# Performance work log

Hardware: AMD Instinct MI355X
Metric: run time of the kernel (lower is better)

## Reference

```python
import jax, jax.numpy as jnp
import numpy as np

N = 100000        # nodes
E = 1600000       # edges (avg degree 16)
IN = 128          # in_channels
HID = 256         # hidden_channels
OUT = 2           # out_channels
G = 512           # num graphs in batch


def setup_inputs() -> dict:
    key = jax.random.key(0)
    ks = jax.random.split(key, 10)
    x = jax.random.normal(ks[0], (N, IN), dtype=jnp.float32)
    edge_index = jax.random.randint(ks[1], (2, E), 0, N, dtype=jnp.int64)
    # sorted graph assignment, every graph non-empty (PyG-style batching)
    batch = (jnp.arange(N, dtype=jnp.int64) * G) // N
    s = 1.0 / np.sqrt(IN)
    sh = 1.0 / np.sqrt(2 * HID)
    sh1 = 1.0 / np.sqrt(HID)
    W_l = jax.random.uniform(ks[2], (HID, IN), jnp.float32, -s, s)   # SAGE lin_l (neighbors)
    b_l = jax.random.uniform(ks[3], (HID,), jnp.float32, -s, s)
    W_r = jax.random.uniform(ks[4], (HID, IN), jnp.float32, -s, s)   # SAGE lin_r (root), no bias
    W0 = jax.random.uniform(ks[5], (HID, IN), jnp.float32, -s, s)    # lin0
    b0 = jax.random.uniform(ks[5], (HID,), jnp.float32, -s, s)
    W1 = jax.random.uniform(ks[6], (HID, 2 * HID), jnp.float32, -sh, sh)  # lin1
    b1 = jax.random.uniform(ks[7], (HID,), jnp.float32, -sh, sh)
    W2 = jax.random.uniform(ks[8], (OUT, HID), jnp.float32, -sh1, sh1)    # lin2
    b2 = jax.random.uniform(ks[9], (OUT,), jnp.float32, -sh1, sh1)
    return {"x": x, "edge_index": edge_index, "batch": batch,
            "W_l": W_l, "b_l": b_l, "W_r": W_r,
            "W0": W0, "b0": b0, "W1": W1, "b1": b1, "W2": W2, "b2": b2}


def reference(x, edge_index, batch, W_l, b_l, W_r, W0, b0, W1, b1, W2, b2):
    src, dst = edge_index[0], edge_index[1]
    # SAGEConv: mean-aggregate neighbor features (gather -> scatter-add -> normalize)
    msg_sum = jax.ops.segment_sum(x[src], dst, num_segments=N)          # [N, IN]
    deg = jax.ops.segment_sum(jnp.ones((E,), x.dtype), dst, num_segments=N)
    aggr = msg_sum / jnp.maximum(deg, 1.0)[:, None]
    h = jax.nn.relu(aggr @ W_l.T + b_l + x @ W_r.T)                     # [N, HID]
    # global max pool per graph
    hp = jax.ops.segment_max(h, batch, num_segments=G)                  # [G, HID]
    # root node = first node of each graph (batch is sorted)
    root = jnp.searchsorted(batch, jnp.arange(G, dtype=batch.dtype))    # [G]
    news = jax.nn.relu(x[root] @ W0.T + b0)                             # [G, HID]
    h = jax.nn.relu(jnp.concatenate([news, hp], axis=-1) @ W1.T + b1)   # [G, HID]
    h = h @ W2.T + b2                                                   # [G, OUT]
    return jax.nn.log_softmax(h, axis=-1)
```

## Files before the change

kernel.cpp:

```cpp
#include <hip/hip_runtime.h>
#include <hip/hip_bf16.h>
#include <math.h>
#include <stdint.h>

#define IN_C 128
#define HID  256
#define OUT_C 2

#define BSHIFT 9
#define BNODES 512
#define EPB 4096

typedef __attribute__((ext_vector_type(8))) short short8;
typedef __attribute__((ext_vector_type(4))) float f32x4;
typedef __attribute__((ext_vector_type(2))) float f32x2;

#if defined(__has_builtin)
#if __has_builtin(__builtin_amdgcn_cvt_pk_f32_fp8) && __has_builtin(__builtin_amdgcn_cvt_pk_fp8_f32)
#define HAVE_FP8_CVT 1
#endif
#if __has_builtin(__builtin_amdgcn_global_load_lds)
#define HAVE_GLL 1
#endif
#endif

__device__ __forceinline__ ushort f2bf(float f) {
  uint32_t u = __float_as_uint(f);
  uint32_t r = u + 0x7FFF + ((u >> 16) & 1);
  return (ushort)(r >> 16);
}
__device__ __forceinline__ float bf2f(ushort b) {
  return __uint_as_float(((uint32_t)b) << 16);
}

#ifndef HAVE_FP8_CVT
__device__ __forceinline__ uint32_t f2fp8_1(float f) {
  uint32_t u = __float_as_uint(f);
  uint32_t s = (u >> 24) & 0x80;
  float a = fabsf(f);
  if (a >= 448.f) return s | 0x7E;
  if (a < 0.015625f) {
    uint32_t m = (uint32_t)(a * 512.f + 0.5f);
    return s | m;
  }
  uint32_t r = u & 0x7fffffff;
  r += 0x7FFFF + ((r >> 20) & 1);
  uint32_t e = (r >> 23) - 127;
  if ((int)e > 8) return s | 0x7E;
  return s | ((e + 7) << 3) | ((r >> 20) & 7);
}
__device__ __forceinline__ float fp8_2f(uint32_t b) {
  uint32_t s = (b & 0x80) << 24;
  uint32_t e = (b >> 3) & 0xF, m = b & 7;
  if (e == 0) { float f = (float)m * 0.001953125f; return s ? -f : f; }
  return __uint_as_float(s | ((e + 120) << 23) | (m << 20));
}
#endif

__device__ __forceinline__ void acc8f8v(f32x2* s, uint2 v) {
#ifdef HAVE_FP8_CVT
  s[0] += __builtin_amdgcn_cvt_pk_f32_fp8(v.x, false);
  s[1] += __builtin_amdgcn_cvt_pk_f32_fp8(v.x, true);
  s[2] += __builtin_amdgcn_cvt_pk_f32_fp8(v.y, false);
  s[3] += __builtin_amdgcn_cvt_pk_f32_fp8(v.y, true);
#else
  s[0].x += fp8_2f(v.x & 0xff);         s[0].y += fp8_2f((v.x >> 8) & 0xff);
  s[1].x += fp8_2f((v.x >> 16) & 0xff); s[1].y += fp8_2f(v.x >> 24);
  s[2].x += fp8_2f(v.y & 0xff);         s[2].y += fp8_2f((v.y >> 8) & 0xff);
  s[3].x += fp8_2f((v.y >> 16) & 0xff); s[3].y += fp8_2f(v.y >> 24);
#endif
}


__global__ void k_hist(const int* __restrict__ dst, int* __restrict__ bcount, int E) {
  __shared__ int h[256];
  int t = threadIdx.x;
  h[t] = 0;
  __syncthreads();
  for (int e = blockIdx.x * 256 + t; e < E; e += gridDim.x * 256)
    atomicAdd(&h[dst[e] >> BSHIFT], 1);
  __syncthreads();
  if (h[t]) atomicAdd(&bcount[t], h[t]);
}

__global__ void k_bucket_scan(const int* __restrict__ bcount,
                              int* __restrict__ bbase, int* __restrict__ bcursor) {
  __shared__ int sd[256];
  int t = threadIdx.x;
  int cnt = bcount[t];
  sd[t] = cnt;
  __syncthreads();
  for (int off = 1; off < 256; off <<= 1) {
    int v = (t >= off) ? sd[t - off] : 0;
    __syncthreads();
    sd[t] += v;
    __syncthreads();
  }
  int base = sd[t] - cnt;
  bbase[t] = base;
  bcursor[t] = base;
}

__global__ __launch_bounds__(256) void k_scatter(
    const int* __restrict__ src, const int* __restrict__ dst,
    int* __restrict__ bcursor, uint32_t* __restrict__ rec, int E) {
  __shared__ int h[256];
  __shared__ int bbase[256];
  __shared__ int lcur[256];
  int t = threadIdx.x;
  int e0 = blockIdx.x * EPB;
  int e1 = e0 + EPB < E ? e0 + EPB : E;
  h[t] = 0; lcur[t] = 0;
  __syncthreads();
  for (int e = e0 + t; e < e1; e += 256)
    atomicAdd(&h[dst[e] >> BSHIFT], 1);
  __syncthreads();
  if (h[t]) bbase[t] = atomicAdd(&bcursor[t], h[t]);
  __syncthreads();
  for (int e = e0 + t; e < e1; e += 256) {
    int d = dst[e];
    int b = d >> BSHIFT;
    int r = atomicAdd(&lcur[b], 1);
    rec[bbase[b] + r] = ((uint32_t)src[e] << BSHIFT) | ((uint32_t)d & (BNODES - 1));
  }
}

__global__ __launch_bounds__(256) void k_csr(
    const uint32_t* __restrict__ rec, const int* __restrict__ bbase,
    const int* __restrict__ bcount,
    int* __restrict__ row_start, int* __restrict__ deg,
    int* __restrict__ csr, int n) {
  __shared__ int ldeg[BNODES];
  __shared__ int lexcl[BNODES];
  __shared__ int ssum[256];
  int t = threadIdx.x;
  int b = blockIdx.x;
  int node0 = b << BSHIFT;
  int ebase = bbase[b];
  int ecnt = bcount[b];

  ldeg[t] = 0; ldeg[t + 256] = 0;
  __syncthreads();
  for (int i = t; i < ecnt; i += 256)
    atomicAdd(&ldeg[rec[ebase + i] & (BNODES - 1)], 1);
  __syncthreads();

  int v0 = ldeg[2 * t], v1 = ldeg[2 * t + 1];
  ssum[t] = v0 + v1;
  __syncthreads();
  for (int off = 1; off < 256; off <<= 1) {
    int v = (t >= off) ? ssum[t - off] : 0;
    __syncthreads();
    ssum[t] += v;
    __syncthreads();
  }
  int excl = ssum[t] - (v0 + v1);
  lexcl[2 * t] = excl;
  lexcl[2 * t + 1] = excl + v0;
  int node = node0 + 2 * t;
  if (node < n) { row_start[node] = ebase + excl; deg[node] = v0; }
  if (node + 1 < n) { row_start[node + 1] = ebase + excl + v0; deg[node + 1] = v1; }
  ldeg[2 * t] = 0; ldeg[2 * t + 1] = 0;
  __syncthreads();
  for (int i = t; i < ecnt; i += 256) {
    uint32_t r = rec[ebase + i];
    int li = r & (BNODES - 1);
    int k = atomicAdd(&ldeg[li], 1);
    csr[ebase + lexcl[li] + k] = (int)(r >> BSHIFT);
  }
}


__global__ void k_prep(const float* __restrict__ x, ushort* __restrict__ xb,
                       uint32_t* __restrict__ xf8, int n4,
                       const float* __restrict__ Wl, const float* __restrict__ Wr,
                       ushort* __restrict__ Wcat,
                       const float* __restrict__ W0, ushort* __restrict__ W0b,
                       const float* __restrict__ W1, ushort* __restrict__ W1b,
                       const int* __restrict__ batch, int* __restrict__ root, int n) {
  int i = blockIdx.x * 256 + threadIdx.x;
  if (i < n4) {
    float4 v = ((const float4*)x)[i];
    ushort4 o = {f2bf(v.x), f2bf(v.y), f2bf(v.z), f2bf(v.w)};
    ((ushort4*)xb)[i] = o;
#ifdef HAVE_FP8_CVT
    int p = __builtin_amdgcn_cvt_pk_fp8_f32(v.x, v.y, 0, false);
    p = __builtin_amdgcn_cvt_pk_fp8_f32(v.z, v.w, p, true);
    xf8[i] = (uint32_t)p;
#else
    xf8[i] = f2fp8_1(v.x) | (f2fp8_1(v.y) << 8) | (f2fp8_1(v.z) << 16) |
             (f2fp8_1(v.w) << 24);
#endif
  }
  if (i < HID * (2 * IN_C) / 4) {
    int c = i >> 6, c4 = (i & 63) * 4;
    float4 v = (c4 < IN_C) ? *(const float4*)(Wl + (size_t)c * IN_C + c4)
                           : *(const float4*)(Wr + (size_t)c * IN_C + (c4 - IN_C));
    ushort4 o = {f2bf(v.x), f2bf(v.y), f2bf(v.z), f2bf(v.w)};
    *(ushort4*)(Wcat + (size_t)c * (2 * IN_C) + c4) = o;
  }
  if (i < HID * IN_C / 4) {
    float4 v = ((const float4*)W0)[i];
    ushort4 o = {f2bf(v.x), f2bf(v.y), f2bf(v.z), f2bf(v.w)};
    ((ushort4*)W0b)[i] = o;
  }
  if (i < HID * 2 * HID / 4) {
    float4 v = ((const float4*)W1)[i];
    ushort4 o = {f2bf(v.x), f2bf(v.y), f2bf(v.z), f2bf(v.w)};
    ((ushort4*)W1b)[i] = o;
  }
  if (i < n) {
    int g = batch[i];
    if (i == 0 || batch[i - 1] != g) root[g] = i;
  }
}


__global__ void k_aggr(const uint32_t* __restrict__ xf8, const int* __restrict__ csr,
                       const int* __restrict__ row_start, const int* __restrict__ deg,
                       ushort* __restrict__ aggr, int n) {
  int wid = threadIdx.x >> 6;
  int lane = threadIdx.x & 63;
  int node = blockIdx.x * 4 + wid;
  if (node >= n) return;
  int base = row_start[node];
  int d = deg[node];
  int q = lane >> 4, li = lane & 15;
  const uint2* xp = (const uint2*)xf8 + li;
  f32x2 s[4] = {};
  int i = q;
  for (; i + 12 < d; i += 16) {
    int n0 = csr[base + i];
    int n1 = csr[base + i + 4];
    int n2 = csr[base + i + 8];
    int n3 = csr[base + i + 12];
    uint2 a = xp[(size_t)n0 * 16];
    uint2 b = xp[(size_t)n1 * 16];
    uint2 c = xp[(size_t)n2 * 16];
    uint2 e = xp[(size_t)n3 * 16];
    acc8f8v(s, a); acc8f8v(s, b); acc8f8v(s, c); acc8f8v(s, e);
  }
  for (; i < d; i += 4) {
    int n0 = csr[base + i];
    uint2 a = xp[(size_t)n0 * 16];
    acc8f8v(s, a);
  }
#pragma unroll
  for (int j = 0; j < 4; ++j) {
    s[j].x += __shfl_xor(s[j].x, 16); s[j].y += __shfl_xor(s[j].y, 16);
    s[j].x += __shfl_xor(s[j].x, 32); s[j].y += __shfl_xor(s[j].y, 32);
  }
  if (q == 0) {
    float inv = 1.0f / (float)(d > 1 ? d : 1);
    uint4 o;
    o.x = (uint32_t)f2bf(s[0].x * inv) | ((uint32_t)f2bf(s[0].y * inv) << 16);
    o.y = (uint32_t)f2bf(s[1].x * inv) | ((uint32_t)f2bf(s[1].y * inv) << 16);
    o.z = (uint32_t)f2bf(s[2].x * inv) | ((uint32_t)f2bf(s[2].y * inv) << 16);
    o.w = (uint32_t)f2bf(s[3].x * inv) | ((uint32_t)f2bf(s[3].y * inv) << 16);
    ((uint4*)(aggr + (size_t)node * IN_C))[li] = o;
  }
}


#ifdef HAVE_GLL
__device__ __forceinline__ void load16_lds(const ushort* g, ushort* l) {
  __builtin_amdgcn_global_load_lds(
      (const __attribute__((address_space(1))) uint32_t*)g,
      (__attribute__((address_space(3))) uint32_t*)l, 16, 0, 0);
}
#endif

__global__ __launch_bounds__(256) void k_gemm_pool(
    const ushort* __restrict__ aggrb, const ushort* __restrict__ xb,
    const ushort* __restrict__ Wcat, const float* __restrict__ bl,
    const int* __restrict__ batch, float* __restrict__ hp, int n) {
  __shared__ ushort sA[64 * 256];
  __shared__ float sbl[256];
  __shared__ int sBatch[64];

  int t = threadIdx.x;
  int n0 = blockIdx.x * 64;
  sbl[t] = bl[t];
  if (t < 64) sBatch[t] = (n0 + t < n) ? batch[n0 + t] : -1;

  int lane = t & 63, w = t >> 6;
  int q = lane >> 4, m = lane & 15;

#pragma unroll
  for (int j = 0; j < 8; ++j) {
    int s = (j * 4 + w) * 64 + lane;
    int r = s >> 5, p = s & 31;
    int c = p ^ (r & 15);
    int gn = n0 + r; gn = gn < n ? gn : n - 1;
    const ushort* g = (c < 16) ? aggrb + (size_t)gn * IN_C + c * 8
                               : xb + (size_t)gn * IN_C + (c - 16) * 8;
#ifdef HAVE_GLL
    load16_lds(g, &sA[(size_t)s * 8]);
#else
    *(uint4*)&sA[(size_t)s * 8] = *(const uint4*)g;
#endif
  }

  short8 bf_n[4];
#pragma unroll
  for (int ct = 0; ct < 4; ++ct)
    bf_n[ct] = *(const short8*)(Wcat + (size_t)(w * 64 + ct * 16 + m) * (2 * IN_C) + q * 8);

  __syncthreads();

  f32x4 acc[4][4] = {};
#pragma unroll
  for (int kc = 0; kc < 8; ++kc) {
    short8 bf[4];
#pragma unroll
    for (int ct = 0; ct < 4; ++ct) bf[ct] = bf_n[ct];
    if (kc < 7) {
#pragma unroll
      for (int ct = 0; ct < 4; ++ct)
        bf_n[ct] = *(const short8*)(Wcat + (size_t)(w * 64 + ct * 16 + m) * (2 * IN_C) +
                                    (kc + 1) * 32 + q * 8);
    }
    short8 af[4];
#pragma unroll
    for (int rt = 0; rt < 4; ++rt) {
      int r = rt * 16 + m;
      int p = (kc * 4 + q) ^ m;
      af[rt] = *(const short8*)&sA[r * 256 + p * 8];
    }
#pragma unroll
    for (int rt = 0; rt < 4; ++rt)
#pragma unroll
      for (int ct = 0; ct < 4; ++ct)
        acc[rt][ct] = __builtin_amdgcn_mfma_f32_16x16x32_bf16(af[rt], bf[ct], acc[rt][ct], 0, 0, 0);
  }

  int last = n - 1 - n0; last = last < 63 ? last : 63;
  int gA = sBatch[0];
  int gB = sBatch[last];
#pragma unroll
  for (int ct = 0; ct < 4; ++ct) {
    int col = w * 64 + ct * 16 + m;
    float bias = sbl[col];
    float mA = 0.f, mB = 0.f;
#pragma unroll
    for (int rt = 0; rt < 4; ++rt) {
#pragma unroll
      for (int i = 0; i < 4; ++i) {
        int lr = rt * 16 + q * 4 + i;
        if (n0 + lr < n) {
          float v = fmaxf(acc[rt][ct][i] + bias, 0.f);
          if (sBatch[lr] == gA) mA = fmaxf(mA, v);
          else mB = fmaxf(mB, v);
        }
      }
    }
    mA = fmaxf(mA, __shfl_xor(mA, 16)); mA = fmaxf(mA, __shfl_xor(mA, 32));
    mB = fmaxf(mB, __shfl_xor(mB, 16)); mB = fmaxf(mB, __shfl_xor(mB, 32));
    if (q == 0) {
      atomicMax((int*)&hp[(size_t)gA * HID + col], __float_as_int(mA));
      if (gB != gA) atomicMax((int*)&hp[(size_t)gB * HID + col], __float_as_int(mB));
    }
  }
}


__global__ __launch_bounds__(256) void k_tail(
    const ushort* __restrict__ xb, const float* __restrict__ hp,
    const int* __restrict__ root,
    const ushort* __restrict__ W0b, const float* __restrict__ b0,
    const ushort* __restrict__ W1b, const float* __restrict__ b1,
    const float* __restrict__ W2, const float* __restrict__ b2,
    float* __restrict__ out, int G) {
  __shared__ ushort sCat[64][264];
  __shared__ int sRoot[64];
  __shared__ float pp[256][2];

  int t = threadIdx.x;
  int g0 = blockIdx.x * 64;
  if (t < 64) sRoot[t] = (g0 + t < G) ? root[g0 + t] : 0;
  __syncthreads();

  int lane = t & 63, w = t >> 6;
  int q = lane >> 4, m = lane & 15;

  const ushort* xrow[4];
#pragma unroll
  for (int rt = 0; rt < 4; ++rt)
    xrow[rt] = xb + (size_t)sRoot[rt * 16 + m] * IN_C;

  {
    f32x4 acc[4][4] = {};
#pragma unroll
    for (int kc = 0; kc < 4; ++kc) {
      short8 af[4], bf[4];
#pragma unroll
      for (int rt = 0; rt < 4; ++rt)
        af[rt] = *(const short8*)(xrow[rt] + kc * 32 + q * 8);
#pragma unroll
      for (int ct = 0; ct < 4; ++ct) {
        int col = w * 64 + ct * 16 + m;
        bf[ct] = *(const short8*)(W0b + (size_t)col * IN_C + kc * 32 + q * 8);
      }
#pragma unroll
      for (int rt = 0; rt < 4; ++rt)
#pragma unroll
        for (int ct = 0; ct < 4; ++ct)
          acc[rt][ct] = __builtin_amdgcn_mfma_f32_16x16x32_bf16(af[rt], bf[ct], acc[rt][ct], 0, 0, 0);
    }
#pragma unroll
    for (int ct = 0; ct < 4; ++ct) {
      int col = w * 64 + ct * 16 + m;
      float bias = b0[col];
#pragma unroll
      for (int rt = 0; rt < 4; ++rt)
#pragma unroll
        for (int i = 0; i < 4; ++i) {
          int row = rt * 16 + q * 4 + i;
          sCat[row][col] = f2bf(fmaxf(acc[rt][ct][i] + bias, 0.f));
        }
    }
  }
  __syncthreads();

  f32x4 acc2[4][4] = {};
#pragma unroll
  for (int kc = 0; kc < 8; ++kc) {
    short8 af[4], bf[4];
#pragma unroll
    for (int rt = 0; rt < 4; ++rt)
      af[rt] = *(const short8*)&sCat[rt * 16 + m][kc * 32 + q * 8];
#pragma unroll
    for (int ct = 0; ct < 4; ++ct) {
      int col = w * 64 + ct * 16 + m;
      bf[ct] = *(const short8*)(W1b + (size_t)col * (2 * HID) + kc * 32 + q * 8);
    }
#pragma unroll
    for (int rt = 0; rt < 4; ++rt)
#pragma unroll
      for (int ct = 0; ct < 4; ++ct)
        acc2[rt][ct] = __builtin_amdgcn_mfma_f32_16x16x32_bf16(af[rt], bf[ct], acc2[rt][ct], 0, 0, 0);
  }
  __syncthreads();
#pragma unroll
  for (int it = 0; it < 16; ++it) {
    int idx = it * 256 + t;
    int r = idx >> 6, c4 = (idx & 63) * 4;
    if (g0 + r < G) {
      float4 v = *(const float4*)(hp + (size_t)(g0 + r) * HID + c4);
      ushort4 o = {f2bf(v.x), f2bf(v.y), f2bf(v.z), f2bf(v.w)};
      *(ushort4*)&sCat[r][c4] = o;
    }
  }
  __syncthreads();
#pragma unroll
  for (int kc = 8; kc < 16; ++kc) {
    short8 af[4], bf[4];
#pragma unroll
    for (int rt = 0; rt < 4; ++rt)
      af[rt] = *(const short8*)&sCat[rt * 16 + m][(kc - 8) * 32 + q * 8];
#pragma unroll
    for (int ct = 0; ct < 4; ++ct) {
      int col = w * 64 + ct * 16 + m;
      bf[ct] = *(const short8*)(W1b + (size_t)col * (2 * HID) + kc * 32 + q * 8);
    }
#pragma unroll
    for (int rt = 0; rt < 4; ++rt)
#pragma unroll
      for (int ct = 0; ct < 4; ++ct)
        acc2[rt][ct] = __builtin_amdgcn_mfma_f32_16x16x32_bf16(af[rt], bf[ct], acc2[rt][ct], 0, 0, 0);
  }
  __syncthreads();
#pragma unroll
  for (int ct = 0; ct < 4; ++ct) {
    int col = w * 64 + ct * 16 + m;
    float bias = b1[col];
#pragma unroll
    for (int rt = 0; rt < 4; ++rt)
#pragma unroll
      for (int i = 0; i < 4; ++i) {
        int row = rt * 16 + q * 4 + i;
        sCat[row][col] = f2bf(fmaxf(acc2[rt][ct][i] + bias, 0.f));
      }
  }
  __syncthreads();

  {
    int row = t >> 2, qq = t & 3;
    float p0 = 0.f, p1 = 0.f;
    for (int c = qq * 64; c < qq * 64 + 64; ++c) {
      float hv = bf2f(sCat[row][c]);
      p0 += hv * W2[c];
      p1 += hv * W2[HID + c];
    }
    pp[t][0] = p0; pp[t][1] = p1;
  }
  __syncthreads();
  if (t < 64 && g0 + t < G) {
    float l0 = b2[0], l1 = b2[1];
#pragma unroll
    for (int k = 0; k < 4; ++k) { l0 += pp[t * 4 + k][0]; l1 += pp[t * 4 + k][1]; }
    float mx = fmaxf(l0, l1);
    float ls = logf(expf(l0 - mx) + expf(l1 - mx));
    out[(size_t)(g0 + t) * 2 + 0] = l0 - mx - ls;
    out[(size_t)(g0 + t) * 2 + 1] = l1 - mx - ls;
  }
}


extern "C" void kernel_launch(void* const* d_in, const int* in_sizes, int n_in,
                              void* d_out, int out_size, void* d_ws, size_t ws_size,
                              hipStream_t stream) {
  const float* x  = (const float*)d_in[0];
  const int* ei   = (const int*)d_in[1];
  const int* batch= (const int*)d_in[2];
  const float* Wl = (const float*)d_in[3];
  const float* bl = (const float*)d_in[4];
  const float* Wr = (const float*)d_in[5];
  const float* W0 = (const float*)d_in[6];
  const float* b0 = (const float*)d_in[7];
  const float* W1 = (const float*)d_in[8];
  const float* b1 = (const float*)d_in[9];
  const float* W2 = (const float*)d_in[10];
  const float* b2 = (const float*)d_in[11];
  float* out = (float*)d_out;

  const int N = in_sizes[0] / IN_C;
  const int E = in_sizes[1] / 2;
  const int G = out_size / OUT_C;
  const int* src = ei;
  const int* dst = ei + E;
  const int NB = (N + BNODES - 1) >> BSHIFT;

  char* w = (char*)d_ws;
  int* deg       = (int*)w; w += (size_t)N * 4;
  int* row_start = (int*)w; w += (size_t)N * 4;
  int* bcount    = (int*)w; w += 1024;
  int* bbase     = (int*)w; w += 1024;
  int* bcursor   = (int*)w; w += 1024;
  int* root      = (int*)w; w += (size_t)G * 4;
  w = (char*)(((uintptr_t)w + 255) & ~(uintptr_t)255);
  int* csr       = (int*)w; w += (size_t)E * 4;
  w = (char*)(((uintptr_t)w + 255) & ~(uintptr_t)255);
  ushort* xb     = (ushort*)w; w += (size_t)N * IN_C * 2;
  uint32_t* xf8  = (uint32_t*)w; w += (size_t)N * IN_C;
  ushort* aggrb  = (ushort*)w; w += (size_t)N * IN_C * 2;
  ushort* Wcat   = (ushort*)w; w += (size_t)HID * (2 * IN_C) * 2;
  ushort* W0b    = (ushort*)w; w += (size_t)HID * IN_C * 2;
  ushort* W1b    = (ushort*)w; w += (size_t)HID * 2 * HID * 2;
  float* hp      = (float*)w; w += (size_t)G * HID * 4;
  uint32_t* rec  = (uint32_t*)aggrb;

  hipMemsetAsync(bcount, 0, 1024, stream);
  hipMemsetAsync(hp, 0, (size_t)G * HID * 4, stream);

  int n4 = N * IN_C / 4;
  k_prep<<<(n4 + 255) / 256, 256, 0, stream>>>(x, xb, xf8, n4, Wl, Wr, Wcat,
                                               W0, W0b, W1, W1b, batch, root, N);
  k_hist<<<1024, 256, 0, stream>>>(dst, bcount, E);
  k_bucket_scan<<<1, 256, 0, stream>>>(bcount, bbase, bcursor);
  k_scatter<<<(E + EPB - 1) / EPB, 256, 0, stream>>>(src, dst, bcursor, rec, E);
  k_csr<<<NB, 256, 0, stream>>>(rec, bbase, bcount, row_start, deg, csr, N);
  k_aggr<<<(N + 3) / 4, 256, 0, stream>>>(xf8, csr, row_start, deg, aggrb, N);
  k_gemm_pool<<<(N + 63) / 64, 256, 0, stream>>>(aggrb, xb, Wcat, bl, batch, hp, N);
  k_tail<<<(G + 63) / 64, 256, 0, stream>>>(xb, hp, root, W0b, b0, W1b, b1, W2, b2, out, G);
}
```

Baseline: 299.9 us.

## Fuse histogram into prep, pad CSR rows, shrink tail tiles

```diff
diff --git a/kernel.cpp b/kernel.cpp
--- a/kernel.cpp
+++ b/kernel.cpp
@@ -7,9 +7,11 @@
 #define HID  256
 #define OUT_C 2
 
-#define BSHIFT 9
-#define BNODES 512
+#define BSHIFT 8
+#define BNODES 256
 #define EPB 4096
+#define HISTB 784
+#define PADB 3840
 
 typedef __attribute__((ext_vector_type(8))) short short8;
 typedef __attribute__((ext_vector_type(4))) float f32x4;
@@ -72,113 +74,18 @@
 }
 
 
-__global__ void k_hist(const int* __restrict__ dst, int* __restrict__ bcount, int E) {
-  __shared__ int h[256];
-  int t = threadIdx.x;
-  h[t] = 0;
-  __syncthreads();
-  for (int e = blockIdx.x * 256 + t; e < E; e += gridDim.x * 256)
-    atomicAdd(&h[dst[e] >> BSHIFT], 1);
-  __syncthreads();
-  if (h[t]) atomicAdd(&bcount[t], h[t]);
-}
-
-__global__ void k_bucket_scan(const int* __restrict__ bcount,
-                              int* __restrict__ bbase, int* __restrict__ bcursor) {
-  __shared__ int sd[256];
-  int t = threadIdx.x;
-  int cnt = bcount[t];
-  sd[t] = cnt;
-  __syncthreads();
-  for (int off = 1; off < 256; off <<= 1) {
-    int v = (t >= off) ? sd[t - off] : 0;
-    __syncthreads();
-    sd[t] += v;
-    __syncthreads();
-  }
-  int base = sd[t] - cnt;
-  bbase[t] = base;
-  bcursor[t] = base;
-}
-
-__global__ __launch_bounds__(256) void k_scatter(
-    const int* __restrict__ src, const int* __restrict__ dst,
-    int* __restrict__ bcursor, uint32_t* __restrict__ rec, int E) {
-  __shared__ int h[256];
-  __shared__ int bbase[256];
-  __shared__ int lcur[256];
-  int t = threadIdx.x;
-  int e0 = blockIdx.x * EPB;
-  int e1 = e0 + EPB < E ? e0 + EPB : E;
-  h[t] = 0; lcur[t] = 0;
-  __syncthreads();
-  for (int e = e0 + t; e < e1; e += 256)
-    atomicAdd(&h[dst[e] >> BSHIFT], 1);
-  __syncthreads();
-  if (h[t]) bbase[t] = atomicAdd(&bcursor[t], h[t]);
-  __syncthreads();
-  for (int e = e0 + t; e < e1; e += 256) {
-    int d = dst[e];
-    int b = d >> BSHIFT;
-    int r = atomicAdd(&lcur[b], 1);
-    rec[bbase[b] + r] = ((uint32_t)src[e] << BSHIFT) | ((uint32_t)d & (BNODES - 1));
-  }
-}
-
-__global__ __launch_bounds__(256) void k_csr(
-    const uint32_t* __restrict__ rec, const int* __restrict__ bbase,
-    const int* __restrict__ bcount,
-    int* __restrict__ row_start, int* __restrict__ deg,
-    int* __restrict__ csr, int n) {
-  __shared__ int ldeg[BNODES];
-  __shared__ int lexcl[BNODES];
-  __shared__ int ssum[256];
-  int t = threadIdx.x;
-  int b = blockIdx.x;
-  int node0 = b << BSHIFT;
-  int ebase = bbase[b];
-  int ecnt = bcount[b];
-
-  ldeg[t] = 0; ldeg[t + 256] = 0;
-  __syncthreads();
-  for (int i = t; i < ecnt; i += 256)
-    atomicAdd(&ldeg[rec[ebase + i] & (BNODES - 1)], 1);
-  __syncthreads();
-
-  int v0 = ldeg[2 * t], v1 = ldeg[2 * t + 1];
-  ssum[t] = v0 + v1;
-  __syncthreads();
-  for (int off = 1; off < 256; off <<= 1) {
-    int v = (t >= off) ? ssum[t - off] : 0;
-    __syncthreads();
-    ssum[t] += v;
-    __syncthreads();
-  }
-  int excl = ssum[t] - (v0 + v1);
-  lexcl[2 * t] = excl;
-  lexcl[2 * t + 1] = excl + v0;
-  int node = node0 + 2 * t;
-  if (node < n) { row_start[node] = ebase + excl; deg[node] = v0; }
-  if (node + 1 < n) { row_start[node + 1] = ebase + excl + v0; deg[node + 1] = v1; }
-  ldeg[2 * t] = 0; ldeg[2 * t + 1] = 0;
-  __syncthreads();
-  for (int i = t; i < ecnt; i += 256) {
-    uint32_t r = rec[ebase + i];
-    int li = r & (BNODES - 1);
-    int k = atomicAdd(&ldeg[li], 1);
-    csr[ebase + lexcl[li] + k] = (int)(r >> BSHIFT);
-  }
-}
-
-
 __global__ void k_prep(const float* __restrict__ x, ushort* __restrict__ xb,
                        uint32_t* __restrict__ xf8, int n4,
                        const float* __restrict__ Wl, const float* __restrict__ Wr,
                        ushort* __restrict__ Wcat,
                        const float* __restrict__ W0, ushort* __restrict__ W0b,
                        const float* __restrict__ W1, ushort* __restrict__ W1b,
-                       const int* __restrict__ batch, int* __restrict__ root, int n) {
-  int i = blockIdx.x * 256 + threadIdx.x;
+                       const int* __restrict__ batch, int* __restrict__ root, int n,
+                       const int* __restrict__ dst, int E, int* __restrict__ bcount,
+                       float* __restrict__ hp, int hp4) {
+  __shared__ int h[512];
+  int t = threadIdx.x;
+  int i = blockIdx.x * 256 + t;
   if (i < n4) {
     float4 v = ((const float4*)x)[i];
     ushort4 o = {f2bf(v.x), f2bf(v.y), f2bf(v.z), f2bf(v.w)};
@@ -192,6 +99,7 @@
              (f2fp8_1(v.w) << 24);
 #endif
   }
+  if (i < 32) xf8[(size_t)n * 32 + i] = 0;
   if (i < HID * (2 * IN_C) / 4) {
     int c = i >> 6, c4 = (i & 63) * 4;
     float4 v = (c4 < IN_C) ? *(const float4*)(Wl + (size_t)c * IN_C + c4)
@@ -209,10 +117,117 @@
     ushort4 o = {f2bf(v.x), f2bf(v.y), f2bf(v.z), f2bf(v.w)};
     ((ushort4*)W1b)[i] = o;
   }
+  if (i < hp4) ((float4*)hp)[i] = make_float4(0.f, 0.f, 0.f, 0.f);
   if (i < n) {
     int g = batch[i];
     if (i == 0 || batch[i - 1] != g) root[g] = i;
   }
+  if (blockIdx.x < HISTB) {
+    h[t] = 0; h[t + 256] = 0;
+    __syncthreads();
+    for (int e = blockIdx.x * 256 + t; e < E; e += HISTB * 256)
+      atomicAdd(&h[dst[e] >> BSHIFT], 1);
+    __syncthreads();
+    if (h[t]) atomicAdd(&bcount[t], h[t]);
+    if (h[t + 256]) atomicAdd(&bcount[t + 256], h[t + 256]);
+  }
+}
+
+
+__global__ __launch_bounds__(256) void k_scatter(
+    const int* __restrict__ src, const int* __restrict__ dst,
+    const int* __restrict__ bcount, int* __restrict__ cursor0,
+    uint32_t* __restrict__ rec, int E) {
+  __shared__ int sBB[512];
+  __shared__ int stmp[256];
+  __shared__ int h[512];
+  __shared__ int hb[512];
+  __shared__ int lcur[512];
+  int t = threadIdx.x;
+  int c0 = bcount[2 * t], c1 = bcount[2 * t + 1];
+  stmp[t] = c0 + c1;
+  h[2 * t] = 0; h[2 * t + 1] = 0;
+  lcur[2 * t] = 0; lcur[2 * t + 1] = 0;
+  __syncthreads();
+  for (int off = 1; off < 256; off <<= 1) {
+    int v = (t >= off) ? stmp[t - off] : 0;
+    __syncthreads();
+    stmp[t] += v;
+    __syncthreads();
+  }
+  int ex = stmp[t] - (c0 + c1);
+  sBB[2 * t] = ex;
+  sBB[2 * t + 1] = ex + c0;
+  __syncthreads();
+
+  int e0 = blockIdx.x * EPB;
+  int e1 = e0 + EPB < E ? e0 + EPB : E;
+  for (int e = e0 + t; e < e1; e += 256)
+    atomicAdd(&h[dst[e] >> BSHIFT], 1);
+  __syncthreads();
+  for (int j = t; j < 512; j += 256)
+    if (h[j]) hb[j] = sBB[j] + atomicAdd(&cursor0[j], h[j]);
+  __syncthreads();
+  for (int e = e0 + t; e < e1; e += 256) {
+    int d = dst[e];
+    int b = d >> BSHIFT;
+    int r = atomicAdd(&lcur[b], 1);
+    rec[hb[b] + r] = ((uint32_t)src[e] << BSHIFT) | ((uint32_t)d & (BNODES - 1));
+  }
+}
+
+
+__global__ __launch_bounds__(256) void k_csr(
+    const uint32_t* __restrict__ rec, const int* __restrict__ bcount,
+    int* __restrict__ row_start, int* __restrict__ deg,
+    int* __restrict__ csr, int n, int zrow) {
+  __shared__ int stmp[256];
+  __shared__ int lexcl[256];
+  __shared__ int ldeg[256];
+  __shared__ int lcur[256];
+  int t = threadIdx.x, b = blockIdx.x;
+  int i2 = 2 * t;
+  int v = ((i2 < b) ? bcount[i2] : 0) + ((i2 + 1 < b) ? bcount[i2 + 1] : 0);
+  stmp[t] = v;
+  ldeg[t] = 0;
+  __syncthreads();
+  for (int off = 128; off > 0; off >>= 1) {
+    if (t < off) stmp[t] += stmp[t + off];
+    __syncthreads();
+  }
+  int ebase = stmp[0];
+  int ecnt = bcount[b];
+  int padbase = ((ebase + 15) & ~15) + PADB * b;
+  int node0 = b << BSHIFT;
+  __syncthreads();
+
+  for (int i = t; i < ecnt; i += 256)
+    atomicAdd(&ldeg[rec[ebase + i] & (BNODES - 1)], 1);
+  __syncthreads();
+  int d = ldeg[t];
+  int P = (d + 15) & ~15;
+  stmp[t] = P;
+  __syncthreads();
+  for (int off = 1; off < 256; off <<= 1) {
+    int vv = (t >= off) ? stmp[t - off] : 0;
+    __syncthreads();
+    stmp[t] += vv;
+    __syncthreads();
+  }
+  int excl = stmp[t] - P;
+  lexcl[t] = excl;
+  int rs = padbase + excl;
+  int node = node0 + t;
+  if (node < n) { row_start[node] = rs; deg[node] = d; }
+  lcur[t] = 0;
+  __syncthreads();
+  for (int i = t; i < ecnt; i += 256) {
+    uint32_t r = rec[ebase + i];
+    int li = r & (BNODES - 1);
+    int k = atomicAdd(&lcur[li], 1);
+    csr[padbase + lexcl[li] + k] = (int)(r >> BSHIFT);
+  }
+  for (int k = d; k < P; ++k) csr[rs + k] = zrow;
 }
 
 
@@ -225,25 +240,17 @@
   if (node >= n) return;
   int base = row_start[node];
   int d = deg[node];
+  int P = (d + 15) & ~15;
   int q = lane >> 4, li = lane & 15;
   const uint2* xp = (const uint2*)xf8 + li;
   f32x2 s[4] = {};
-  int i = q;
-  for (; i + 12 < d; i += 16) {
-    int n0 = csr[base + i];
-    int n1 = csr[base + i + 4];
-    int n2 = csr[base + i + 8];
-    int n3 = csr[base + i + 12];
-    uint2 a = xp[(size_t)n0 * 16];
-    uint2 b = xp[(size_t)n1 * 16];
-    uint2 c = xp[(size_t)n2 * 16];
-    uint2 e = xp[(size_t)n3 * 16];
+  for (int i = 4 * q; i < P; i += 16) {
+    int4 ns = *(const int4*)(csr + base + i);
+    uint2 a = xp[(size_t)ns.x * 16];
+    uint2 b = xp[(size_t)ns.y * 16];
+    uint2 c = xp[(size_t)ns.z * 16];
+    uint2 e = xp[(size_t)ns.w * 16];
     acc8f8v(s, a); acc8f8v(s, b); acc8f8v(s, c); acc8f8v(s, e);
-  }
-  for (; i < d; i += 4) {
-    int n0 = csr[base + i];
-    uint2 a = xp[(size_t)n0 * 16];
-    acc8f8v(s, a);
   }
 #pragma unroll
   for (int j = 0; j < 4; ++j) {
@@ -371,30 +378,30 @@
     const ushort* __restrict__ W1b, const float* __restrict__ b1,
     const float* __restrict__ W2, const float* __restrict__ b2,
     float* __restrict__ out, int G) {
-  __shared__ ushort sCat[64][264];
-  __shared__ int sRoot[64];
+  __shared__ ushort sCat[32][264];
+  __shared__ int sRoot[32];
   __shared__ float pp[256][2];
 
   int t = threadIdx.x;
-  int g0 = blockIdx.x * 64;
-  if (t < 64) sRoot[t] = (g0 + t < G) ? root[g0 + t] : 0;
+  int g0 = blockIdx.x * 32;
+  if (t < 32) sRoot[t] = (g0 + t < G) ? root[g0 + t] : 0;
   __syncthreads();
 
   int lane = t & 63, w = t >> 6;
   int q = lane >> 4, m = lane & 15;
 
-  const ushort* xrow[4];
-#pragma unroll
-  for (int rt = 0; rt < 4; ++rt)
+  const ushort* xrow[2];
+#pragma unroll
+  for (int rt = 0; rt < 2; ++rt)
     xrow[rt] = xb + (size_t)sRoot[rt * 16 + m] * IN_C;
 
   {
-    f32x4 acc[4][4] = {};
+    f32x4 acc[2][4] = {};
 #pragma unroll
     for (int kc = 0; kc < 4; ++kc) {
-      short8 af[4], bf[4];
-#pragma unroll
-      for (int rt = 0; rt < 4; ++rt)
+      short8 af[2], bf[4];
+#pragma unroll
+      for (int rt = 0; rt < 2; ++rt)
         af[rt] = *(const short8*)(xrow[rt] + kc * 32 + q * 8);
 #pragma unroll
       for (int ct = 0; ct < 4; ++ct) {
@@ -402,7 +409,7 @@
         bf[ct] = *(const short8*)(W0b + (size_t)col * IN_C + kc * 32 + q * 8);
       }
 #pragma unroll
-      for (int rt = 0; rt < 4; ++rt)
+      for (int rt = 0; rt < 2; ++rt)
 #pragma unroll
         for (int ct = 0; ct < 4; ++ct)
           acc[rt][ct] = __builtin_amdgcn_mfma_f32_16x16x32_bf16(af[rt], bf[ct], acc[rt][ct], 0, 0, 0);
@@ -412,7 +419,7 @@
       int col = w * 64 + ct * 16 + m;
       float bias = b0[col];
 #pragma unroll
-      for (int rt = 0; rt < 4; ++rt)
+      for (int rt = 0; rt < 2; ++rt)
 #pragma unroll
         for (int i = 0; i < 4; ++i) {
           int row = rt * 16 + q * 4 + i;
@@ -422,27 +429,34 @@
   }
   __syncthreads();
 
-  f32x4 acc2[4][4] = {};
+  f32x4 acc2[2][4] = {};
+  short8 bfn[4];
+#pragma unroll
+  for (int ct = 0; ct < 4; ++ct)
+    bfn[ct] = *(const short8*)(W1b + (size_t)(w * 64 + ct * 16 + m) * (2 * HID) + q * 8);
 #pragma unroll
   for (int kc = 0; kc < 8; ++kc) {
-    short8 af[4], bf[4];
-#pragma unroll
-    for (int rt = 0; rt < 4; ++rt)
+    short8 af[2], bf[4];
+#pragma unroll
+    for (int ct = 0; ct < 4; ++ct) bf[ct] = bfn[ct];
+    if (kc < 7) {
+#pragma unroll
+      for (int ct = 0; ct < 4; ++ct)
+        bfn[ct] = *(const short8*)(W1b + (size_t)(w * 64 + ct * 16 + m) * (2 * HID) +
+                                   (kc + 1) * 32 + q * 8);
+    }
+#pragma unroll
+    for (int rt = 0; rt < 2; ++rt)
       af[rt] = *(const short8*)&sCat[rt * 16 + m][kc * 32 + q * 8];
 #pragma unroll
-    for (int ct = 0; ct < 4; ++ct) {
-      int col = w * 64 + ct * 16 + m;
-      bf[ct] = *(const short8*)(W1b + (size_t)col * (2 * HID) + kc * 32 + q * 8);
-    }
-#pragma unroll
-    for (int rt = 0; rt < 4; ++rt)
+    for (int rt = 0; rt < 2; ++rt)
 #pragma unroll
       for (int ct = 0; ct < 4; ++ct)
         acc2[rt][ct] = __builtin_amdgcn_mfma_f32_16x16x32_bf16(af[rt], bf[ct], acc2[rt][ct], 0, 0, 0);
   }
   __syncthreads();
 #pragma unroll
-  for (int it = 0; it < 16; ++it) {
+  for (int it = 0; it < 8; ++it) {
     int idx = it * 256 + t;
     int r = idx >> 6, c4 = (idx & 63) * 4;
     if (g0 + r < G) {
@@ -453,18 +467,24 @@
   }
   __syncthreads();
 #pragma unroll
+  for (int ct = 0; ct < 4; ++ct)
+    bfn[ct] = *(const short8*)(W1b + (size_t)(w * 64 + ct * 16 + m) * (2 * HID) + 8 * 32 + q * 8);
+#pragma unroll
   for (int kc = 8; kc < 16; ++kc) {
-    short8 af[4], bf[4];
-#pragma unroll
-    for (int rt = 0; rt < 4; ++rt)
+    short8 af[2], bf[4];
+#pragma unroll
+    for (int ct = 0; ct < 4; ++ct) bf[ct] = bfn[ct];
+    if (kc < 15) {
+#pragma unroll
+      for (int ct = 0; ct < 4; ++ct)
+        bfn[ct] = *(const short8*)(W1b + (size_t)(w * 64 + ct * 16 + m) * (2 * HID) +
+                                   (kc + 1) * 32 + q * 8);
+    }
+#pragma unroll
+    for (int rt = 0; rt < 2; ++rt)
       af[rt] = *(const short8*)&sCat[rt * 16 + m][(kc - 8) * 32 + q * 8];
 #pragma unroll
-    for (int ct = 0; ct < 4; ++ct) {
-      int col = w * 64 + ct * 16 + m;
-      bf[ct] = *(const short8*)(W1b + (size_t)col * (2 * HID) + kc * 32 + q * 8);
-    }
-#pragma unroll
-    for (int rt = 0; rt < 4; ++rt)
+    for (int rt = 0; rt < 2; ++rt)
 #pragma unroll
       for (int ct = 0; ct < 4; ++ct)
         acc2[rt][ct] = __builtin_amdgcn_mfma_f32_16x16x32_bf16(af[rt], bf[ct], acc2[rt][ct], 0, 0, 0);
@@ -475,7 +495,7 @@
     int col = w * 64 + ct * 16 + m;
     float bias = b1[col];
 #pragma unroll
-    for (int rt = 0; rt < 4; ++rt)
+    for (int rt = 0; rt < 2; ++rt)
 #pragma unroll
       for (int i = 0; i < 4; ++i) {
         int row = rt * 16 + q * 4 + i;
@@ -485,9 +505,9 @@
   __syncthreads();
 
   {
-    int row = t >> 2, qq = t & 3;
+    int row = t >> 3, qq = t & 7;
     float p0 = 0.f, p1 = 0.f;
-    for (int c = qq * 64; c < qq * 64 + 64; ++c) {
+    for (int c = qq * 32; c < qq * 32 + 32; ++c) {
       float hv = bf2f(sCat[row][c]);
       p0 += hv * W2[c];
       p1 += hv * W2[HID + c];
@@ -495,10 +515,10 @@
     pp[t][0] = p0; pp[t][1] = p1;
   }
   __syncthreads();
-  if (t < 64 && g0 + t < G) {
+  if (t < 32 && g0 + t < G) {
     float l0 = b2[0], l1 = b2[1];
 #pragma unroll
-    for (int k = 0; k < 4; ++k) { l0 += pp[t * 4 + k][0]; l1 += pp[t * 4 + k][1]; }
+    for (int k = 0; k < 8; ++k) { l0 += pp[t * 8 + k][0]; l1 += pp[t * 8 + k][1]; }
     float mx = fmaxf(l0, l1);
     float ls = logf(expf(l0 - mx) + expf(l1 - mx));
     out[(size_t)(g0 + t) * 2 + 0] = l0 - mx - ls;
@@ -534,15 +554,14 @@
   char* w = (char*)d_ws;
   int* deg       = (int*)w; w += (size_t)N * 4;
   int* row_start = (int*)w; w += (size_t)N * 4;
-  int* bcount    = (int*)w; w += 1024;
-  int* bbase     = (int*)w; w += 1024;
-  int* bcursor   = (int*)w; w += 1024;
+  int* bcount    = (int*)w; w += 2048;
+  int* cursor0   = (int*)w; w += 2048;
   int* root      = (int*)w; w += (size_t)G * 4;
   w = (char*)(((uintptr_t)w + 255) & ~(uintptr_t)255);
-  int* csr       = (int*)w; w += (size_t)E * 4;
+  int* csr       = (int*)w; w += (size_t)(E + PADB * NB + 8192) * 4;
   w = (char*)(((uintptr_t)w + 255) & ~(uintptr_t)255);
   ushort* xb     = (ushort*)w; w += (size_t)N * IN_C * 2;
-  uint32_t* xf8  = (uint32_t*)w; w += (size_t)N * IN_C;
+  uint32_t* xf8  = (uint32_t*)w; w += (size_t)(N + 1) * IN_C;
   ushort* aggrb  = (ushort*)w; w += (size_t)N * IN_C * 2;
   ushort* Wcat   = (ushort*)w; w += (size_t)HID * (2 * IN_C) * 2;
   ushort* W0b    = (ushort*)w; w += (size_t)HID * IN_C * 2;
@@ -550,17 +569,15 @@
   float* hp      = (float*)w; w += (size_t)G * HID * 4;
   uint32_t* rec  = (uint32_t*)aggrb;
 
-  hipMemsetAsync(bcount, 0, 1024, stream);
-  hipMemsetAsync(hp, 0, (size_t)G * HID * 4, stream);
+  hipMemsetAsync(bcount, 0, 4096, stream);
 
   int n4 = N * IN_C / 4;
-  k_prep<<<(n4 + 255) / 256, 256, 0, stream>>>(x, xb, xf8, n4, Wl, Wr, Wcat,
-                                               W0, W0b, W1, W1b, batch, root, N);
-  k_hist<<<1024, 256, 0, stream>>>(dst, bcount, E);
-  k_bucket_scan<<<1, 256, 0, stream>>>(bcount, bbase, bcursor);
-  k_scatter<<<(E + EPB - 1) / EPB, 256, 0, stream>>>(src, dst, bcursor, rec, E);
-  k_csr<<<NB, 256, 0, stream>>>(rec, bbase, bcount, row_start, deg, csr, N);
+  k_prep<<<(n4 + 255) / 256, 256, 0, stream>>>(
+      x, xb, xf8, n4, Wl, Wr, Wcat, W0, W0b, W1, W1b, batch, root, N,
+      dst, E, bcount, hp, G * HID / 4);
+  k_scatter<<<(E + EPB - 1) / EPB, 256, 0, stream>>>(src, dst, bcount, cursor0, rec, E);
+  k_csr<<<NB, 256, 0, stream>>>(rec, bcount, row_start, deg, csr, N, N);
   k_aggr<<<(N + 3) / 4, 256, 0, stream>>>(xf8, csr, row_start, deg, aggrb, N);
   k_gemm_pool<<<(N + 63) / 64, 256, 0, stream>>>(aggrb, xb, Wcat, bl, batch, hp, N);
-  k_tail<<<(G + 63) / 64, 256, 0, stream>>>(xb, hp, root, W0b, b0, W1b, b1, W2, b2, out, G);
-}
+  k_tail<<<(G + 31) / 32, 256, 0, stream>>>(xb, hp, root, W0b, b0, W1b, b1, W2, b2, out, G);
+}
```

After: 274.8 us. -8.4%, faster.
